# Kernel optimization log

Measured on AMD Instinct MI355X. Metric: run time of the kernel, lower is better.

The kernel has to match this reference:

```python
import jax, jax.numpy as jnp
import numpy as np

N_USER = 50000
N_ITEM = 50000
E = 500000
D = 256
H = 8
DK = D // H
EPS = 1e-5
SQRT_DK = float(np.sqrt(DK))


def _layernorm(x, g, b):
    m = jnp.mean(x, axis=-1, keepdims=True)
    v = jnp.var(x, axis=-1, keepdims=True)
    return (x - m) * jax.lax.rsqrt(v + EPS) * g + b


def _etype_aggregate(h_src, h_dst, src, dst, n_dst, Wk, bk, Wq, bq, Wv, bv, pri, att, msg):
    # per-ntype K/Q/V projections, then per-relation head-wise transforms
    k = (h_src @ Wk + bk).reshape(-1, H, DK)
    v = (h_src @ Wv + bv).reshape(-1, H, DK)
    q = (h_dst @ Wq + bq).reshape(-1, H, DK)
    k = jnp.einsum('nhi,hij->nhj', k, att)
    v = jnp.einsum('nhi,hij->nhj', v, msg)
    # v_dot_u score per edge per head: [E, H]
    score = jnp.einsum('ehd,ehd->eh', q[dst], k[src]) * pri / SQRT_DK
    # edge_softmax normalized per destination node (per head)
    smax = jax.ops.segment_max(score, dst, num_segments=n_dst)
    ex = jnp.exp(score - smax[dst])
    ssum = jax.ops.segment_sum(ex, dst, num_segments=n_dst)
    a = ex / ssum[dst]
    # u_mul_e + sum reduce (zero-in-degree dst nodes get zeros, like DGL sum)
    t = jax.ops.segment_sum(v[src] * a[:, :, None], dst, num_segments=n_dst)
    return t.reshape(n_dst, D)


def _dst_update(t, h, Wa, ba, skip, g, b):
    alpha = jax.nn.sigmoid(skip)
    out = (t @ Wa + ba) * alpha + h * (1.0 - alpha)
    return _layernorm(out, g, b)


def _forward(h_user, h_item, src_ui, dst_ui, src_iu, dst_iu, Wk_user, bk_user, Wq_user, bq_user, Wv_user, bv_user, Wa_user, ba_user, ln_g_user, ln_b_user, skip_user, Wk_item, bk_item, Wq_item, bq_item, Wv_item, bv_item, Wa_item, ba_item, ln_g_item, ln_b_item, skip_item, pri_ui, att_ui, msg_ui, pri_iu, att_iu, msg_iu):
    # (user, click, item): k/v from src ntype 'user', q from dst ntype 'item'
    t_item = _etype_aggregate(h_user, h_item, src_ui, dst_ui, N_ITEM, Wk_user, bk_user, Wq_item, bq_item, Wv_user, bv_user, pri_ui, att_ui, msg_ui)
    # (item, rev_click, user)
    t_user = _etype_aggregate(h_item, h_user, src_iu, dst_iu, N_USER, Wk_item, bk_item, Wq_user, bq_user, Wv_item, bv_item, pri_iu, att_iu, msg_iu)
    # each ntype is dst of exactly one etype -> cross_reducer 'mean' is identity
    new_user = _dst_update(t_user, h_user, Wa_user, ba_user, skip_user, ln_g_user, ln_b_user)
    new_item = _dst_update(t_item, h_item, Wa_item, ba_item, skip_item, ln_g_item, ln_b_item)
    return jnp.stack([new_user, new_item])  # [2, N, D]


def setup_inputs() -> dict:
    key = jax.random.key(0)
    ks = jax.random.split(key, 16)

    def xavier(k, shape):
        s = np.sqrt(2.0 / (shape[-2] + shape[-1]))
        return (jax.random.normal(k, shape, dtype=jnp.float32) * s).astype(jnp.float32)

    inp = {}
    inp['h_user'] = jax.random.normal(ks[0], (N_USER, D), dtype=jnp.float32)
    inp['h_item'] = jax.random.normal(ks[1], (N_ITEM, D), dtype=jnp.float32)
    inp['src_ui'] = jax.random.randint(ks[2], (E,), 0, N_USER, dtype=jnp.int32)
    inp['dst_ui'] = jax.random.randint(ks[3], (E,), 0, N_ITEM, dtype=jnp.int32)
    inp['src_iu'] = jax.random.randint(ks[4], (E,), 0, N_ITEM, dtype=jnp.int32)
    inp['dst_iu'] = jax.random.randint(ks[5], (E,), 0, N_USER, dtype=jnp.int32)
    i = 6
    for nt in ['user', 'item']:
        for nm in ['k', 'q', 'v', 'a']:
            inp[f'W{nm}_{nt}'] = xavier(jax.random.fold_in(ks[i], hash(nm) % 1000), (D, D))
            inp[f'b{nm}_{nt}'] = jnp.zeros((D,), jnp.float32)
        i += 1
        inp[f'ln_g_{nt}'] = jnp.ones((D,), jnp.float32)
        inp[f'ln_b_{nt}'] = jnp.zeros((D,), jnp.float32)
        inp[f'skip_{nt}'] = jnp.ones((1,), jnp.float32)
    for et in ['ui', 'iu']:
        inp[f'pri_{et}'] = jnp.ones((H,), jnp.float32)
        inp[f'att_{et}'] = xavier(ks[i], (H, DK, DK)); i += 1
        inp[f'msg_{et}'] = xavier(ks[i], (H, DK, DK)); i += 1
    return inp


def reference(h_user, h_item, src_ui, dst_ui, src_iu, dst_iu, Wk_user, bk_user, Wq_user, bq_user, Wv_user, bv_user, Wa_user, ba_user, ln_g_user, ln_b_user, skip_user, Wk_item, bk_item, Wq_item, bq_item, Wv_item, bv_item, Wa_item, ba_item, ln_g_item, ln_b_item, skip_item, pri_ui, att_ui, msg_ui, pri_iu, att_iu, msg_iu):
    return _forward(h_user, h_item, src_ui, dst_ui, src_iu, dst_iu, Wk_user, bk_user, Wq_user, bq_user, Wv_user, bv_user, Wa_user, ba_user, ln_g_user, ln_b_user, skip_user, Wk_item, bk_item, Wq_item, bq_item, Wv_item, bv_item, Wa_item, ba_item, ln_g_item, ln_b_item, skip_item, pri_ui, att_ui, msg_ui, pri_iu, att_iu, msg_iu)
```

## Files before the change

kernel.cpp:

```cpp
#include <hip/hip_runtime.h>

#define NN 50000
#define DD 256
#define HH 8
#define EE 500000
#define INV_SQRT_DK 0.17677669529663687f

typedef __attribute__((ext_vector_type(8))) short bf16x8;
typedef __attribute__((ext_vector_type(4))) float f32x4;

__device__ __forceinline__ unsigned short f2bf(float f) {
    unsigned int u = __float_as_uint(f);
    u = (u + 0x7FFFu + ((u >> 16) & 1u)) >> 16;
    return (unsigned short)u;
}
__device__ __forceinline__ float bf2f(unsigned short u) {
    return __uint_as_float(((unsigned int)u) << 16);
}
__device__ __forceinline__ float bflo(unsigned int u) {
    return __uint_as_float(u << 16);
}
__device__ __forceinline__ float bfhi(unsigned int u) {
    return __uint_as_float(u & 0xFFFF0000u);
}

__global__ __launch_bounds__(256) void conv_hist(const float* __restrict__ Xu,
                                                 const float* __restrict__ Xi,
                                                 unsigned short* __restrict__ Yu,
                                                 unsigned short* __restrict__ Yi,
                                                 const int* __restrict__ dst_ui,
                                                 const int* __restrict__ dst_iu,
                                                 int* __restrict__ cnt) {
    int bx = blockIdx.x;
    if (bx < 25000) {
        const size_t ND = (size_t)NN * DD;
        size_t i = ((size_t)bx * 256 + threadIdx.x) * 4;
        const float* X = Xu; unsigned short* Y = Yu;
        if (i >= ND) { X = Xi; Y = Yi; i -= ND; }
        float4 v = *(const float4*)&X[i];
        ushort4 o;
        o.x = f2bf(v.x); o.y = f2bf(v.y); o.z = f2bf(v.z); o.w = f2bf(v.w);
        *(ushort4*)&Y[i] = o;
    } else {
        int e = (bx - 25000) * 256 + threadIdx.x;
        if (e < EE) atomicAdd(&cnt[dst_ui[e]], 1);
        else if (e < 2 * EE) atomicAdd(&cnt[NN + dst_iu[e - EE]], 1);
    }
}

__global__ __launch_bounds__(256) void weights_kernel(const float* __restrict__ Wk_u, const float* __restrict__ bk_u,
                                                      const float* __restrict__ att_ui_,
                                                      const float* __restrict__ Wv_u, const float* __restrict__ bv_u,
                                                      const float* __restrict__ msg_ui_,
                                                      const float* __restrict__ Wk_i, const float* __restrict__ bk_i,
                                                      const float* __restrict__ att_iu_,
                                                      const float* __restrict__ Wv_i, const float* __restrict__ bv_i,
                                                      const float* __restrict__ msg_iu_,
                                                      const float* __restrict__ Wq_u, const float* __restrict__ bq_u,
                                                      const float* __restrict__ Wq_i, const float* __restrict__ bq_i,
                                                      const float* __restrict__ Wa_u, const float* __restrict__ Wa_i,
                                                      unsigned short* __restrict__ BTu, float* __restrict__ beffU,
                                                      unsigned short* __restrict__ BTi, float* __restrict__ beffI,
                                                      unsigned short* __restrict__ WaTu, unsigned short* __restrict__ WaTi) {
    int y = blockIdx.y;
    if (y < 4) {
        const float* W = (y == 0) ? Wk_u : (y == 1) ? Wv_u : (y == 2) ? Wk_i : Wv_i;
        const float* b = (y == 0) ? bk_u : (y == 1) ? bv_u : (y == 2) ? bk_i : bv_i;
        const float* T = (y == 0) ? att_ui_ : (y == 1) ? msg_ui_ : (y == 2) ? att_iu_ : msg_iu_;
        unsigned short* WT = (y < 2) ? BTu : BTi;
        float* be = (y < 2) ? beffU : beffI;
        int j = threadIdx.x;
        int h = j >> 5, jj = j & 31;
        int pj = ((j >> 2) << 3) + (j & 3) + ((y & 1) ? 4 : 0);
        const float* Th = T + h * 1024;
        if (blockIdx.x < 256) {
            int c = blockIdx.x;
            float acc = 0.f;
            #pragma unroll 8
            for (int i = 0; i < 32; ++i) acc += W[c * 256 + h * 32 + i] * Th[i * 32 + jj];
            WT[pj * 256 + c] = f2bf(acc);
        } else {
            float acc = 0.f;
            #pragma unroll 8
            for (int i = 0; i < 32; ++i) acc += b[h * 32 + i] * Th[i * 32 + jj];
            be[pj] = acc;
        }
    } else if (blockIdx.x < 256) {
        int yy = y - 4;
        const float* W = (yy == 0) ? Wq_u : (yy == 1) ? Wq_i : (yy == 2) ? Wa_u : Wa_i;
        unsigned short* WT = (yy == 0) ? BTu + 512 * 256 : (yy == 1) ? BTi + 512 * 256 : (yy == 2) ? WaTu : WaTi;
        int k = blockIdx.x, n = threadIdx.x;
        WT[n * 256 + k] = f2bf(W[k * 256 + n]);
        if (k == 0 && yy < 2) {
            float* be = (yy == 0) ? beffU : beffI;
            const float* bq = (yy == 0) ? bq_u : bq_i;
            be[512 + n] = bq[n];
        }
    }
}

__global__ __launch_bounds__(256) void alloc_kernel(const int* __restrict__ cnt,
                                                    int* __restrict__ start,
                                                    int* __restrict__ ctr) {
    int y = blockIdx.y;
    int i = blockIdx.x * 256 + threadIdx.x;
    int idx = y * NN + i;
    int v = (i < NN) ? cnt[idx] : 0;
    int lane = threadIdx.x & 63;
    int pre = v;
    #pragma unroll
    for (int o = 1; o < 64; o <<= 1) {
        int u = __shfl_up(pre, o, 64);
        if (lane >= o) pre += u;
    }
    int wsum = __shfl(pre, 63, 64);
    int base = 0;
    if (lane == 63) base = atomicAdd(&ctr[y], wsum);
    base = __shfl(base, 63, 64);
    if (i < NN) start[idx] = y * EE + base + pre - v;
}

__global__ void scatter_kernel(const int* __restrict__ dst_ui, const int* __restrict__ src_ui,
                               const int* __restrict__ dst_iu, const int* __restrict__ src_iu,
                               const int* __restrict__ start, int* __restrict__ cur,
                               unsigned short* __restrict__ srcid) {
    int e = blockIdx.x * blockDim.x + threadIdx.x;
    int d, s;
    if (e < EE) { d = dst_ui[e]; s = src_ui[e]; }
    else if (e < 2 * EE) { d = NN + dst_iu[e - EE]; s = src_iu[e - EE]; }
    else return;
    int pos = start[d] + atomicAdd(&cur[d], 1);
    srcid[pos] = (unsigned short)s;
}

__global__ __launch_bounds__(256) void gemm_kvq(const unsigned short* __restrict__ Au,
                                                const unsigned short* __restrict__ Ai,
                                                const unsigned short* __restrict__ BTu,
                                                const unsigned short* __restrict__ BTi,
                                                const float* __restrict__ beffU,
                                                const float* __restrict__ beffI,
                                                unsigned short* __restrict__ KVu,
                                                unsigned short* __restrict__ KVi,
                                                unsigned short* __restrict__ Qu,
                                                unsigned short* __restrict__ Qi) {
    __shared__ __align__(16) char smem[40960];
    bf16x8* As0 = (bf16x8*)smem;
    bf16x8* Bs0 = (bf16x8*)(smem + 10240);
    bf16x8* As1 = (bf16x8*)(smem + 20480);
    bf16x8* Bs1 = (bf16x8*)(smem + 30720);
    int bsw = blockIdx.x;
    int xcd = bsw & 7, sidx = bsw >> 3;
    int wg = (xcd < 4 ? xcd * 587 : 2348 + (xcd - 4) * 586) + sidx;
    int bni = wg % 6; int rest = wg / 6;
    int bmi = rest % 391; int z = rest / 391;
    const unsigned short* A = z ? Ai : Au;
    const unsigned short* BT = z ? BTi : BTu;
    const float* beff = z ? beffI : beffU;
    unsigned short* KV = z ? KVi : KVu;
    unsigned short* Qb = z ? Qi : Qu;
    int bm = bmi * 128, bn = bni * 128;
    int tid = threadIdx.x;
    int lane = tid & 63, w = tid >> 6;
    int wm = (w & 1) * 64, wn = (w >> 1) * 64;
    int m16 = lane & 15, q = lane >> 4;

    int row0 = tid >> 2, off = tid & 3;
    int row1 = row0 + 64;
    int gr0 = bm + row0, gr1 = bm + row1;
    const bool val0 = gr0 < NN, val1 = gr1 < NN;
    const unsigned short* pA0 = &A[(size_t)gr0 * 256 + off * 8];
    const unsigned short* pA1 = &A[(size_t)gr1 * 256 + off * 8];
    const unsigned short* pB0 = &BT[(size_t)(bn + row0) * 256 + off * 8];
    const unsigned short* pB1 = &BT[(size_t)(bn + row1) * 256 + off * 8];

    f32x4 acc[4][4] = {};
    const bf16x8 zz = {};
    bf16x8 ra0 = zz, ra1 = zz, rb0, rb1;
    if (val0) ra0 = *(const bf16x8*)pA0;
    if (val1) ra1 = *(const bf16x8*)pA1;
    rb0 = *(const bf16x8*)pB0;
    rb1 = *(const bf16x8*)pB1;
    As0[row0 * 5 + off] = ra0; As0[row1 * 5 + off] = ra1;
    Bs0[row0 * 5 + off] = rb0; Bs0[row1 * 5 + off] = rb1;
    ra0 = zz; ra1 = zz;
    if (val0) ra0 = *(const bf16x8*)(pA0 + 32);
    if (val1) ra1 = *(const bf16x8*)(pA1 + 32);
    rb0 = *(const bf16x8*)(pB0 + 32);
    rb1 = *(const bf16x8*)(pB1 + 32);
    __syncthreads();
    #pragma unroll
    for (int ks = 0; ks < 8; ++ks) {
        bf16x8* Ac = (ks & 1) ? As1 : As0;
        bf16x8* Bc = (ks & 1) ? Bs1 : Bs0;
        bf16x8* An = (ks & 1) ? As0 : As1;
        bf16x8* Bn = (ks & 1) ? Bs0 : Bs1;
        if (ks < 7) {
            An[row0 * 5 + off] = ra0; An[row1 * 5 + off] = ra1;
            Bn[row0 * 5 + off] = rb0; Bn[row1 * 5 + off] = rb1;
        }
        if (ks < 6) {
            int k0 = (ks + 2) * 32;
            ra0 = zz; ra1 = zz;
            if (val0) ra0 = *(const bf16x8*)(pA0 + k0);
            if (val1) ra1 = *(const bf16x8*)(pA1 + k0);
            rb0 = *(const bf16x8*)(pB0 + k0);
            rb1 = *(const bf16x8*)(pB1 + k0);
        }
        bf16x8 af[4], bfr[4];
        #pragma unroll
        for (int i = 0; i < 4; ++i) af[i] = Ac[(wm + 16 * i + m16) * 5 + q];
        #pragma unroll
        for (int j = 0; j < 4; ++j) bfr[j] = Bc[(wn + 16 * j + m16) * 5 + q];
        #pragma unroll
        for (int i = 0; i < 4; ++i)
            #pragma unroll
            for (int j = 0; j < 4; ++j)
                acc[i][j] = __builtin_amdgcn_mfma_f32_16x16x32_bf16(af[i], bfr[j], acc[i][j], 0, 0, 0);
        __syncthreads();
    }
    const bool isKV = (bn < 512);
    unsigned short* dstb = isKV ? KV : Qb;
    const int rowlen = isKV ? 512 : 256;
    const int coloff = isKV ? bn : (bn - 512);
    unsigned short* Cs = (unsigned short*)smem;
    #pragma unroll
    for (int half = 0; half < 2; ++half) {
        if ((w & 1) == half) {
            #pragma unroll
            for (int i = 0; i < 4; ++i) {
                int rloc = 16 * i + q * 4;
                #pragma unroll
                for (int j = 0; j < 4; ++j) {
                    int cl = wn + 16 * j + m16;
                    float bv = beff[bn + cl];
                    #pragma unroll
                    for (int r = 0; r < 4; ++r)
                        Cs[(rloc + r) * 136 + cl] = f2bf(acc[i][j][r] + bv);
                }
            }
        }
        __syncthreads();
        #pragma unroll
        for (int it = 0; it < 4; ++it) {
            int idx = it * 256 + tid;
            int row = idx >> 4, seg = idx & 15;
            int gr = bm + half * 64 + row;
            if (gr < NN) {
                bf16x8 v = *(const bf16x8*)&Cs[row * 136 + seg * 8];
                *(bf16x8*)&dstb[(size_t)gr * rowlen + coloff + seg * 8] = v;
            }
        }
        __syncthreads();
    }
}

__global__ __launch_bounds__(512) void gemm_ln(const unsigned short* __restrict__ A0,
                                               const unsigned short* __restrict__ A1,
                                               const unsigned short* __restrict__ BT0,
                                               const unsigned short* __restrict__ BT1,
                                               const float* __restrict__ ba0,
                                               const float* __restrict__ ba1,
                                               const float* __restrict__ h0,
                                               const float* __restrict__ h1,
                                               const float* __restrict__ skp0,
                                               const float* __restrict__ skp1,
                                               const float* __restrict__ g0, const float* __restrict__ be0,
                                               const float* __restrict__ g1, const float* __restrict__ be1,
                                               float* __restrict__ out) {
    __shared__ __align__(16) char smem[33280];
    bf16x8* As = (bf16x8*)smem;
    bf16x8* Bs = (bf16x8*)(smem + 10240);
    float* Es = (float*)smem;
    int z = blockIdx.y;
    const unsigned short* A = z ? A1 : A0;
    const unsigned short* BT = z ? BT1 : BT0;
    const float* ba = z ? ba1 : ba0;
    const float* hb = z ? h1 : h0;
    const float* skp = z ? skp1 : skp0;
    const float* g = z ? g1 : g0;
    const float* bb = z ? be1 : be0;
    float* o = out + (z ? (size_t)NN * DD : 0);

    int bm = blockIdx.x * 128;
    int tid = threadIdx.x;
    int lane = tid & 63, w = tid >> 6;
    int m16 = lane & 15, q = lane >> 4;
    f32x4 acc[16] = {};
    for (int k0 = 0; k0 < 256; k0 += 32) {
        {
            int row = tid >> 2, ch = tid & 3;
            int gr = bm + row;
            bf16x8 va = {};
            if (gr < NN) va = *(const bf16x8*)&A[(size_t)gr * 256 + k0 + ch * 8];
            As[row * 5 + ch] = va;
        }
        #pragma unroll
        for (int cc = 0; cc < 2; ++cc) {
            int idx = tid + cc * 512;
            int n = idx >> 2, ch = idx & 3;
            Bs[n * 5 + ch] = *(const bf16x8*)&BT[(size_t)n * 256 + k0 + ch * 8];
        }
        __syncthreads();
        bf16x8 af = As[(w * 16 + m16) * 5 + q];
        #pragma unroll
        for (int jh = 0; jh < 2; ++jh) {
            bf16x8 bfr[8];
            #pragma unroll
            for (int jj = 0; jj < 8; ++jj) bfr[jj] = Bs[((jh * 8 + jj) * 16 + m16) * 5 + q];
            #pragma unroll
            for (int jj = 0; jj < 8; ++jj)
                acc[jh * 8 + jj] = __builtin_amdgcn_mfma_f32_16x16x32_bf16(af, bfr[jj], acc[jh * 8 + jj], 0, 0, 0);
        }
        __syncthreads();
    }
    float alpha = 1.f / (1.f + __expf(-skp[0]));
    float am1 = 1.f - alpha;
    float4 ba4 = *(const float4*)&ba[lane * 4];
    float4 g4 = *(const float4*)&g[lane * 4];
    float4 b4 = *(const float4*)&bb[lane * 4];
    #pragma unroll
    for (int p = 0; p < 4; ++p) {
        if ((w >> 1) == p) {
            int rbase = (w & 1) * 16 + 4 * q;
            #pragma unroll
            for (int j = 0; j < 16; ++j)
                #pragma unroll
                for (int rr = 0; rr < 4; ++rr)
                    Es[(rbase + rr) * 260 + 16 * j + m16] = acc[j][rr];
        }
        __syncthreads();
        #pragma unroll
        for (int rrr = 0; rrr < 4; ++rrr) {
            int lrow = w * 4 + rrr;
            int gr = bm + 32 * p + lrow;
            if (gr < NN) {
                float4 tm = *(const float4*)&Es[lrow * 260 + lane * 4];
                float4 hh = *(const float4*)&hb[(size_t)gr * 256 + lane * 4];
                float x0 = (tm.x + ba4.x) * alpha + hh.x * am1;
                float x1 = (tm.y + ba4.y) * alpha + hh.y * am1;
                float x2 = (tm.z + ba4.z) * alpha + hh.z * am1;
                float x3 = (tm.w + ba4.w) * alpha + hh.w * am1;
                float s = x0 + x1 + x2 + x3;
                #pragma unroll
                for (int off = 32; off > 0; off >>= 1) s += __shfl_xor(s, off, 64);
                float mean = s * (1.f / 256.f);
                float d0 = x0 - mean, d1 = x1 - mean, d2 = x2 - mean, d3 = x3 - mean;
                float s2 = d0 * d0 + d1 * d1 + d2 * d2 + d3 * d3;
                #pragma unroll
                for (int off = 32; off > 0; off >>= 1) s2 += __shfl_xor(s2, off, 64);
                float rstd = rsqrtf(s2 * (1.f / 256.f) + 1e-5f);
                float4 r;
                r.x = d0 * rstd * g4.x + b4.x;
                r.y = d1 * rstd * g4.y + b4.y;
                r.z = d2 * rstd * g4.z + b4.z;
                r.w = d3 * rstd * g4.w + b4.w;
                *(float4*)&o[(size_t)gr * 256 + lane * 4] = r;
            }
        }
        __syncthreads();
    }
}

__global__ __launch_bounds__(256) void fused_agg(const int* __restrict__ start,
                                                 const int* __restrict__ cnt,
                                                 const unsigned short* __restrict__ srcid,
                                                 const unsigned short* __restrict__ Qi,
                                                 const unsigned short* __restrict__ Qu,
                                                 const unsigned short* __restrict__ KVu,
                                                 const unsigned short* __restrict__ KVi,
                                                 const float* __restrict__ pri_ui,
                                                 const float* __restrict__ pri_iu,
                                                 unsigned short* __restrict__ tI16,
                                                 unsigned short* __restrict__ tU16) {
    int w = threadIdx.x >> 6;
    int lane = threadIdx.x & 63;
    int b = blockIdx.x * 4 + w;
    bool second = (b >= NN);
    int d = second ? b - NN : b;
    const unsigned short* Q = second ? Qu : Qi;
    const unsigned short* KV = second ? KVi : KVu;
    const float* pri = second ? pri_iu : pri_ui;
    unsigned short* T = second ? tU16 : tI16;

    int h = lane >> 3;
    float sscale = pri[h] * INV_SQRT_DK;
    ushort4 q4 = *(const ushort4*)&Q[(size_t)d * 256 + lane * 4];
    float qx = bf2f(q4.x), qy = bf2f(q4.y), qz = bf2f(q4.z), qw = bf2f(q4.w);

    int p0 = start[b], n = cnt[b];
    float a0 = 0.f, a1 = 0.f, a2 = 0.f, a3 = 0.f, l = 0.f;

#define LDKV(idx) (*(const uint4*)&KV[(size_t)__shfl(myS, (idx), 64) * 512 + lane * 8])
#define PROC(kv) { \
        float sc = qx * bflo(kv.x) + qy * bfhi(kv.x) + qz * bflo(kv.y) + qw * bfhi(kv.y); \
        sc += __shfl_xor(sc, 1, 8); \
        sc += __shfl_xor(sc, 2, 8); \
        sc += __shfl_xor(sc, 4, 8); \
        float wgt = __expf(sc * sscale); \
        a0 += wgt * bflo(kv.z); \
        a1 += wgt * bfhi(kv.z); \
        a2 += wgt * bflo(kv.w); \
        a3 += wgt * bfhi(kv.w); \
        l += wgt; }

    for (int base = 0; base < n; base += 64) {
        int rem = n - base; if (rem > 64) rem = 64;
        int myS = (lane < rem) ? (int)srcid[p0 + base + lane] : 0;
        uint4 k0 = {}, k1 = {}, k2 = {}, k3 = {};
        if (0 < rem) k0 = LDKV(0);
        if (1 < rem) k1 = LDKV(1);
        if (2 < rem) k2 = LDKV(2);
        if (3 < rem) k3 = LDKV(3);
        int t = 0;
        for (; t + 4 <= rem; t += 4) {
            PROC(k0); if (t + 4 < rem) k0 = LDKV(t + 4);
            PROC(k1); if (t + 5 < rem) k1 = LDKV(t + 5);
            PROC(k2); if (t + 6 < rem) k2 = LDKV(t + 6);
            PROC(k3); if (t + 7 < rem) k3 = LDKV(t + 7);
        }
        if (t < rem)     PROC(k0);
        if (t + 1 < rem) PROC(k1);
        if (t + 2 < rem) PROC(k2);
    }
#undef LDKV
#undef PROC

    float inv = (l > 0.f) ? 1.f / l : 0.f;
    ushort4 o;
    o.x = f2bf(a0 * inv); o.y = f2bf(a1 * inv);
    o.z = f2bf(a2 * inv); o.w = f2bf(a3 * inv);
    *(ushort4*)&T[(size_t)d * 256 + lane * 4] = o;
}

extern "C" void kernel_launch(void* const* d_in, const int* in_sizes, int n_in,
                              void* d_out, int out_size, void* d_ws, size_t ws_size,
                              hipStream_t stream) {
    const float* h_user  = (const float*)d_in[0];
    const float* h_item  = (const float*)d_in[1];
    const int*   src_ui  = (const int*)d_in[2];
    const int*   dst_ui  = (const int*)d_in[3];
    const int*   src_iu  = (const int*)d_in[4];
    const int*   dst_iu  = (const int*)d_in[5];
    const float* Wk_user = (const float*)d_in[6];
    const float* bk_user = (const float*)d_in[7];
    const float* Wq_user = (const float*)d_in[8];
    const float* bq_user = (const float*)d_in[9];
    const float* Wv_user = (const float*)d_in[10];
    const float* bv_user = (const float*)d_in[11];
    const float* Wa_user = (const float*)d_in[12];
    const float* ba_user = (const float*)d_in[13];
    const float* ln_g_user = (const float*)d_in[14];
    const float* ln_b_user = (const float*)d_in[15];
    const float* skip_user = (const float*)d_in[16];
    const float* Wk_item = (const float*)d_in[17];
    const float* bk_item = (const float*)d_in[18];
    const float* Wq_item = (const float*)d_in[19];
    const float* bq_item = (const float*)d_in[20];
    const float* Wv_item = (const float*)d_in[21];
    const float* bv_item = (const float*)d_in[22];
    const float* Wa_item = (const float*)d_in[23];
    const float* ba_item = (const float*)d_in[24];
    const float* ln_g_item = (const float*)d_in[25];
    const float* ln_b_item = (const float*)d_in[26];
    const float* skip_item = (const float*)d_in[27];
    const float* pri_ui = (const float*)d_in[28];
    const float* att_ui = (const float*)d_in[29];
    const float* msg_ui = (const float*)d_in[30];
    const float* pri_iu = (const float*)d_in[31];
    const float* att_iu = (const float*)d_in[32];
    const float* msg_iu = (const float*)d_in[33];
    float* out = (float*)d_out;

    const size_t ND = (size_t)NN * DD;

    unsigned short* up = (unsigned short*)d_ws;
    unsigned short* KVu = up;  up += (size_t)NN * 512;
    unsigned short* KVi = up;  up += (size_t)NN * 512;
    unsigned short* Qu  = up;  up += ND;
    unsigned short* Qi  = up;  up += ND;
    unsigned short* hU16 = up; up += ND;
    unsigned short* hI16 = up; up += ND;
    unsigned short* BTu = up;  up += 768 * 256;
    unsigned short* BTi = up;  up += 768 * 256;
    unsigned short* WaTu = up; up += 65536;
    unsigned short* WaTi = up; up += 65536;
    float* fp = (float*)up;
    float* beffU = fp; fp += 768;
    float* beffI = fp; fp += 768;
    int* ip = (int*)fp;
    int* cnt   = ip; ip += 2 * NN;
    int* cur   = ip; ip += 2 * NN;
    int* ctr   = ip; ip += 2;
    int* start = ip; ip += 2 * NN;
    unsigned short* srcid = (unsigned short*)ip;
    unsigned short* tU16 = hU16;
    unsigned short* tI16 = hI16;

    const int eb = (EE + 255) / 256;

    hipMemsetAsync(cnt, 0, (4 * NN + 2) * sizeof(int), stream);
    conv_hist<<<25000 + 2 * eb, 256, 0, stream>>>(h_user, h_item, hU16, hI16,
                                                  dst_ui, dst_iu, cnt);
    weights_kernel<<<dim3(257, 8), 256, 0, stream>>>(Wk_user, bk_user, att_ui, Wv_user, bv_user, msg_ui,
                                                     Wk_item, bk_item, att_iu, Wv_item, bv_item, msg_iu,
                                                     Wq_user, bq_user, Wq_item, bq_item, Wa_user, Wa_item,
                                                     BTu, beffU, BTi, beffI, WaTu, WaTi);
    alloc_kernel<<<dim3(196, 2), 256, 0, stream>>>(cnt, start, ctr);
    scatter_kernel<<<2 * eb, 256, 0, stream>>>(dst_ui, src_ui, dst_iu, src_iu, start, cur, srcid);

    gemm_kvq<<<4692, 256, 0, stream>>>(hU16, hI16, BTu, BTi, beffU, beffI,
                                       KVu, KVi, Qu, Qi);

    fused_agg<<<25000, 256, 0, stream>>>(start, cnt, srcid, Qi, Qu, KVu, KVi,
                                         pri_ui, pri_iu, tI16, tU16);

    gemm_ln<<<dim3(391, 2), 512, 0, stream>>>(tU16, tI16, WaTu, WaTi, ba_user, ba_item,
                                              h_user, h_item, skip_user, skip_item,
                                              ln_g_user, ln_b_user, ln_g_item, ln_b_item, out);
}
```

Before: 646.9 us.

## Fuse fp32-to-bf16 input conversion into K/V/Q GEMM A-tile loads

Drops the standalone pass that converted h_user/h_item to bf16 and has the projection GEMM read fp32 rows directly, packing them to bf16 before the shared-memory store. The weight preparation and degree histogram are merged into a single prep kernel, removing one launch. The GEMM prefetch is restructured with two register stages to hide the larger fp32 loads. This removes a full write and re-read of 2x50000x256 bf16 data, but each GEMM tile now reads twice the A bytes and the 6 N-blocks per row each re-read the fp32 rows.

```diff
diff --git a/kernel.cpp b/kernel.cpp
--- a/kernel.cpp
+++ b/kernel.cpp
@@ -23,46 +23,39 @@
 __device__ __forceinline__ float bfhi(unsigned int u) {
     return __uint_as_float(u & 0xFFFF0000u);
 }
-
-__global__ __launch_bounds__(256) void conv_hist(const float* __restrict__ Xu,
-                                                 const float* __restrict__ Xi,
-                                                 unsigned short* __restrict__ Yu,
-                                                 unsigned short* __restrict__ Yi,
-                                                 const int* __restrict__ dst_ui,
-                                                 const int* __restrict__ dst_iu,
-                                                 int* __restrict__ cnt) {
-    int bx = blockIdx.x;
-    if (bx < 25000) {
-        const size_t ND = (size_t)NN * DD;
-        size_t i = ((size_t)bx * 256 + threadIdx.x) * 4;
-        const float* X = Xu; unsigned short* Y = Yu;
-        if (i >= ND) { X = Xi; Y = Yi; i -= ND; }
-        float4 v = *(const float4*)&X[i];
-        ushort4 o;
-        o.x = f2bf(v.x); o.y = f2bf(v.y); o.z = f2bf(v.z); o.w = f2bf(v.w);
-        *(ushort4*)&Y[i] = o;
-    } else {
-        int e = (bx - 25000) * 256 + threadIdx.x;
+__device__ __forceinline__ bf16x8 pack8(float4 lo, float4 hi) {
+    bf16x8 v;
+    v[0] = (short)f2bf(lo.x); v[1] = (short)f2bf(lo.y);
+    v[2] = (short)f2bf(lo.z); v[3] = (short)f2bf(lo.w);
+    v[4] = (short)f2bf(hi.x); v[5] = (short)f2bf(hi.y);
+    v[6] = (short)f2bf(hi.z); v[7] = (short)f2bf(hi.w);
+    return v;
+}
+
+__global__ __launch_bounds__(256) void prep_kernel(const float* __restrict__ Wk_u, const float* __restrict__ bk_u,
+                                                   const float* __restrict__ att_ui_,
+                                                   const float* __restrict__ Wv_u, const float* __restrict__ bv_u,
+                                                   const float* __restrict__ msg_ui_,
+                                                   const float* __restrict__ Wk_i, const float* __restrict__ bk_i,
+                                                   const float* __restrict__ att_iu_,
+                                                   const float* __restrict__ Wv_i, const float* __restrict__ bv_i,
+                                                   const float* __restrict__ msg_iu_,
+                                                   const float* __restrict__ Wq_u, const float* __restrict__ bq_u,
+                                                   const float* __restrict__ Wq_i, const float* __restrict__ bq_i,
+                                                   const float* __restrict__ Wa_u, const float* __restrict__ Wa_i,
+                                                   unsigned short* __restrict__ BTu, float* __restrict__ beffU,
+                                                   unsigned short* __restrict__ BTi, float* __restrict__ beffI,
+                                                   unsigned short* __restrict__ WaTu, unsigned short* __restrict__ WaTi,
+                                                   const int* __restrict__ dst_ui, const int* __restrict__ dst_iu,
+                                                   int* __restrict__ cnt) {
+    int blk = blockIdx.x;
+    if (blk >= 2056) {
+        int e = (blk - 2056) * 256 + threadIdx.x;
         if (e < EE) atomicAdd(&cnt[dst_ui[e]], 1);
         else if (e < 2 * EE) atomicAdd(&cnt[NN + dst_iu[e - EE]], 1);
-    }
-}
-
-__global__ __launch_bounds__(256) void weights_kernel(const float* __restrict__ Wk_u, const float* __restrict__ bk_u,
-                                                      const float* __restrict__ att_ui_,
-                                                      const float* __restrict__ Wv_u, const float* __restrict__ bv_u,
-                                                      const float* __restrict__ msg_ui_,
-                                                      const float* __restrict__ Wk_i, const float* __restrict__ bk_i,
-                                                      const float* __restrict__ att_iu_,
-                                                      const float* __restrict__ Wv_i, const float* __restrict__ bv_i,
-                                                      const float* __restrict__ msg_iu_,
-                                                      const float* __restrict__ Wq_u, const float* __restrict__ bq_u,
-                                                      const float* __restrict__ Wq_i, const float* __restrict__ bq_i,
-                                                      const float* __restrict__ Wa_u, const float* __restrict__ Wa_i,
-                                                      unsigned short* __restrict__ BTu, float* __restrict__ beffU,
-                                                      unsigned short* __restrict__ BTi, float* __restrict__ beffI,
-                                                      unsigned short* __restrict__ WaTu, unsigned short* __restrict__ WaTi) {
-    int y = blockIdx.y;
+        return;
+    }
+    int y = blk / 257, x = blk % 257;
     if (y < 4) {
         const float* W = (y == 0) ? Wk_u : (y == 1) ? Wv_u : (y == 2) ? Wk_i : Wv_i;
         const float* b = (y == 0) ? bk_u : (y == 1) ? bv_u : (y == 2) ? bk_i : bv_i;
@@ -73,8 +66,8 @@
         int h = j >> 5, jj = j & 31;
         int pj = ((j >> 2) << 3) + (j & 3) + ((y & 1) ? 4 : 0);
         const float* Th = T + h * 1024;
-        if (blockIdx.x < 256) {
-            int c = blockIdx.x;
+        if (x < 256) {
+            int c = x;
             float acc = 0.f;
             #pragma unroll 8
             for (int i = 0; i < 32; ++i) acc += W[c * 256 + h * 32 + i] * Th[i * 32 + jj];
@@ -85,11 +78,11 @@
             for (int i = 0; i < 32; ++i) acc += b[h * 32 + i] * Th[i * 32 + jj];
             be[pj] = acc;
         }
-    } else if (blockIdx.x < 256) {
+    } else if (x < 256) {
         int yy = y - 4;
         const float* W = (yy == 0) ? Wq_u : (yy == 1) ? Wq_i : (yy == 2) ? Wa_u : Wa_i;
         unsigned short* WT = (yy == 0) ? BTu + 512 * 256 : (yy == 1) ? BTi + 512 * 256 : (yy == 2) ? WaTu : WaTi;
-        int k = blockIdx.x, n = threadIdx.x;
+        int k = x, n = threadIdx.x;
         WT[n * 256 + k] = f2bf(W[k * 256 + n]);
         if (k == 0 && yy < 2) {
             float* be = (yy == 0) ? beffU : beffI;
@@ -133,8 +126,8 @@
     srcid[pos] = (unsigned short)s;
 }
 
-__global__ __launch_bounds__(256) void gemm_kvq(const unsigned short* __restrict__ Au,
-                                                const unsigned short* __restrict__ Ai,
+__global__ __launch_bounds__(256) void gemm_kvq(const float* __restrict__ Hu,
+                                                const float* __restrict__ Hi,
                                                 const unsigned short* __restrict__ BTu,
                                                 const unsigned short* __restrict__ BTi,
                                                 const float* __restrict__ beffU,
@@ -153,7 +146,7 @@
     int wg = (xcd < 4 ? xcd * 587 : 2348 + (xcd - 4) * 586) + sidx;
     int bni = wg % 6; int rest = wg / 6;
     int bmi = rest % 391; int z = rest / 391;
-    const unsigned short* A = z ? Ai : Au;
+    const float* H = z ? Hi : Hu;
     const unsigned short* BT = z ? BTi : BTu;
     const float* beff = z ? beffI : beffU;
     unsigned short* KV = z ? KVi : KVu;
@@ -168,56 +161,63 @@
     int row1 = row0 + 64;
     int gr0 = bm + row0, gr1 = bm + row1;
     const bool val0 = gr0 < NN, val1 = gr1 < NN;
-    const unsigned short* pA0 = &A[(size_t)gr0 * 256 + off * 8];
-    const unsigned short* pA1 = &A[(size_t)gr1 * 256 + off * 8];
+    const float* pA0 = &H[(size_t)gr0 * 256 + off * 8];
+    const float* pA1 = &H[(size_t)gr1 * 256 + off * 8];
     const unsigned short* pB0 = &BT[(size_t)(bn + row0) * 256 + off * 8];
     const unsigned short* pB1 = &BT[(size_t)(bn + row1) * 256 + off * 8];
 
     f32x4 acc[4][4] = {};
-    const bf16x8 zz = {};
-    bf16x8 ra0 = zz, ra1 = zz, rb0, rb1;
-    if (val0) ra0 = *(const bf16x8*)pA0;
-    if (val1) ra1 = *(const bf16x8*)pA1;
-    rb0 = *(const bf16x8*)pB0;
-    rb1 = *(const bf16x8*)pB1;
-    As0[row0 * 5 + off] = ra0; As0[row1 * 5 + off] = ra1;
-    Bs0[row0 * 5 + off] = rb0; Bs0[row1 * 5 + off] = rb1;
-    ra0 = zz; ra1 = zz;
-    if (val0) ra0 = *(const bf16x8*)(pA0 + 32);
-    if (val1) ra1 = *(const bf16x8*)(pA1 + 32);
-    rb0 = *(const bf16x8*)(pB0 + 32);
-    rb1 = *(const bf16x8*)(pB1 + 32);
+    const float4 zf = {0.f, 0.f, 0.f, 0.f};
+    float4 Al0A, Ah0A, Al1A, Ah1A; bf16x8 B0A, B1A;
+    float4 Al0B, Ah0B, Al1B, Ah1B; bf16x8 B0B, B1B;
+
+#define LDA(S, kt) { \
+        Al0##S = zf; Ah0##S = zf; Al1##S = zf; Ah1##S = zf; \
+        if (val0) { Al0##S = *(const float4*)(pA0 + (kt) * 32); \
+                    Ah0##S = *(const float4*)(pA0 + (kt) * 32 + 4); } \
+        if (val1) { Al1##S = *(const float4*)(pA1 + (kt) * 32); \
+                    Ah1##S = *(const float4*)(pA1 + (kt) * 32 + 4); } \
+        B0##S = *(const bf16x8*)(pB0 + (kt) * 32); \
+        B1##S = *(const bf16x8*)(pB1 + (kt) * 32); }
+
+#define WRS(Adst, Bdst, S) { \
+        Adst[row0 * 5 + off] = pack8(Al0##S, Ah0##S); \
+        Adst[row1 * 5 + off] = pack8(Al1##S, Ah1##S); \
+        Bdst[row0 * 5 + off] = B0##S; \
+        Bdst[row1 * 5 + off] = B1##S; }
+
+#define ITER(ks, S) { \
+        bf16x8* Ac = ((ks) & 1) ? As1 : As0; \
+        bf16x8* Bc = ((ks) & 1) ? Bs1 : Bs0; \
+        if ((ks) < 7) { \
+            bf16x8* An = ((ks) & 1) ? As0 : As1; \
+            bf16x8* Bn = ((ks) & 1) ? Bs0 : Bs1; \
+            WRS(An, Bn, S); \
+        } \
+        if ((ks) < 5) LDA(S, (ks) + 3); \
+        bf16x8 af[4], bfr[4]; \
+        _Pragma("unroll") \
+        for (int i = 0; i < 4; ++i) af[i] = Ac[(wm + 16 * i + m16) * 5 + q]; \
+        _Pragma("unroll") \
+        for (int j = 0; j < 4; ++j) bfr[j] = Bc[(wn + 16 * j + m16) * 5 + q]; \
+        _Pragma("unroll") \
+        for (int i = 0; i < 4; ++i) \
+            _Pragma("unroll") \
+            for (int j = 0; j < 4; ++j) \
+                acc[i][j] = __builtin_amdgcn_mfma_f32_16x16x32_bf16(af[i], bfr[j], acc[i][j], 0, 0, 0); \
+        __syncthreads(); }
+
+    LDA(A, 0)
+    WRS(As0, Bs0, A)
+    LDA(A, 1)
+    LDA(B, 2)
     __syncthreads();
-    #pragma unroll
-    for (int ks = 0; ks < 8; ++ks) {
-        bf16x8* Ac = (ks & 1) ? As1 : As0;
-        bf16x8* Bc = (ks & 1) ? Bs1 : Bs0;
-        bf16x8* An = (ks & 1) ? As0 : As1;
-        bf16x8* Bn = (ks & 1) ? Bs0 : Bs1;
-        if (ks < 7) {
-            An[row0 * 5 + off] = ra0; An[row1 * 5 + off] = ra1;
-            Bn[row0 * 5 + off] = rb0; Bn[row1 * 5 + off] = rb1;
-        }
-        if (ks < 6) {
-            int k0 = (ks + 2) * 32;
-            ra0 = zz; ra1 = zz;
-            if (val0) ra0 = *(const bf16x8*)(pA0 + k0);
-            if (val1) ra1 = *(const bf16x8*)(pA1 + k0);
-            rb0 = *(const bf16x8*)(pB0 + k0);
-            rb1 = *(const bf16x8*)(pB1 + k0);
-        }
-        bf16x8 af[4], bfr[4];
-        #pragma unroll
-        for (int i = 0; i < 4; ++i) af[i] = Ac[(wm + 16 * i + m16) * 5 + q];
-        #pragma unroll
-        for (int j = 0; j < 4; ++j) bfr[j] = Bc[(wn + 16 * j + m16) * 5 + q];
-        #pragma unroll
-        for (int i = 0; i < 4; ++i)
-            #pragma unroll
-            for (int j = 0; j < 4; ++j)
-                acc[i][j] = __builtin_amdgcn_mfma_f32_16x16x32_bf16(af[i], bfr[j], acc[i][j], 0, 0, 0);
-        __syncthreads();
-    }
+    ITER(0, A) ITER(1, B) ITER(2, A) ITER(3, B)
+    ITER(4, A) ITER(5, B) ITER(6, A) ITER(7, B)
+#undef LDA
+#undef WRS
+#undef ITER
+
     const bool isKV = (bn < 512);
     unsigned short* dstb = isKV ? KV : Qb;
     const int rowlen = isKV ? 512 : 256;
@@ -478,8 +478,8 @@
     unsigned short* KVi = up;  up += (size_t)NN * 512;
     unsigned short* Qu  = up;  up += ND;
     unsigned short* Qi  = up;  up += ND;
-    unsigned short* hU16 = up; up += ND;
-    unsigned short* hI16 = up; up += ND;
+    unsigned short* tU16 = up; up += ND;
+    unsigned short* tI16 = up; up += ND;
     unsigned short* BTu = up;  up += 768 * 256;
     unsigned short* BTi = up;  up += 768 * 256;
     unsigned short* WaTu = up; up += 65536;
@@ -493,22 +493,19 @@
     int* ctr   = ip; ip += 2;
     int* start = ip; ip += 2 * NN;
     unsigned short* srcid = (unsigned short*)ip;
-    unsigned short* tU16 = hU16;
-    unsigned short* tI16 = hI16;
 
     const int eb = (EE + 255) / 256;
 
     hipMemsetAsync(cnt, 0, (4 * NN + 2) * sizeof(int), stream);
-    conv_hist<<<25000 + 2 * eb, 256, 0, stream>>>(h_user, h_item, hU16, hI16,
-                                                  dst_ui, dst_iu, cnt);
-    weights_kernel<<<dim3(257, 8), 256, 0, stream>>>(Wk_user, bk_user, att_ui, Wv_user, bv_user, msg_ui,
-                                                     Wk_item, bk_item, att_iu, Wv_item, bv_item, msg_iu,
-                                                     Wq_user, bq_user, Wq_item, bq_item, Wa_user, Wa_item,
-                                                     BTu, beffU, BTi, beffI, WaTu, WaTi);
+    prep_kernel<<<2056 + 2 * eb, 256, 0, stream>>>(Wk_user, bk_user, att_ui, Wv_user, bv_user, msg_ui,
+                                                   Wk_item, bk_item, att_iu, Wv_item, bv_item, msg_iu,
+                                                   Wq_user, bq_user, Wq_item, bq_item, Wa_user, Wa_item,
+                                                   BTu, beffU, BTi, beffI, WaTu, WaTi,
+                                                   dst_ui, dst_iu, cnt);
     alloc_kernel<<<dim3(196, 2), 256, 0, stream>>>(cnt, start, ctr);
     scatter_kernel<<<2 * eb, 256, 0, stream>>>(dst_ui, src_ui, dst_iu, src_iu, start, cur, srcid);
 
-    gemm_kvq<<<4692, 256, 0, stream>>>(hU16, hI16, BTu, BTi, beffU, beffI,
+    gemm_kvq<<<4692, 256, 0, stream>>>(h_user, h_item, BTu, BTi, beffU, beffI,
                                        KVu, KVi, Qu, Qi);
 
     fused_agg<<<25000, 256, 0, stream>>>(start, cnt, srcid, Qi, Qu, KVu, KVi,
```

Measured after the change: 663.1 us. +2.5%, slower.
